# Optimization experiments

Measured on AMD Instinct MI355X. Metric: run time of the kernel, lower is better.

## Reference

```python
import jax, jax.numpy as jnp
import numpy as np


def setup_inputs() -> dict:
    key = jax.random.key(0)
    k1, k2 = jax.random.split(key)
    B, C, T = 16, 256, 1500
    K = 2048
    x = jax.random.normal(k1, (B, C, T), dtype=jnp.float32)
    # torch init: uniform(-1/K, 1/K)
    codebook = jax.random.uniform(k2, (K, C), dtype=jnp.float32,
                                  minval=-1.0 / K, maxval=1.0 / K)
    return {"x": x, "codebook": codebook}


def reference(x, codebook):
    B, C, T = x.shape
    # (B, T, C) -> (B*T, C)
    x_flat = jnp.transpose(x, (0, 2, 1)).reshape(-1, C)
    distances = (jnp.sum(x_flat * x_flat, axis=1, keepdims=True)
                 - 2.0 * x_flat @ codebook.T
                 + jnp.sum(codebook * codebook, axis=1))  # (B*T, K)
    indices = jnp.argmin(distances, axis=1)               # (B*T,)
    quantized_flat = codebook[indices]                    # (B*T, C)
    quantized = jnp.transpose(quantized_flat.reshape(B, T, C), (0, 2, 1))
    indices_out = indices.reshape(B, 1, T)
    # straight-through estimator
    quantized_out = x + jax.lax.stop_gradient(quantized - x)
    commitment_loss = jnp.mean((jax.lax.stop_gradient(quantized) - x) ** 2)
    return quantized_out, indices_out, commitment_loss
```

## Files before the change

kernel.cpp:

```cpp
#include <hip/hip_runtime.h>


#define B_DIM 16
#define C_DIM 256
#define T_DIM 1500
#define K_CODES 2048
#define N_ROWS (B_DIM * T_DIM)
#define TOTAL_ELEMS (B_DIM * C_DIM * T_DIM)

#define TM 32
#define TKC 256
#define CS 32
#define OT 64

__global__ __launch_bounds__(256) void vq_se(const float* __restrict__ cb,
                                             float* __restrict__ Se) {
    const int k = blockIdx.x * 256 + threadIdx.x;
    if (k >= K_CODES) return;
    const float* row = cb + (size_t)k * C_DIM;
    float h[2];
#pragma unroll
    for (int half = 0; half < 2; ++half) {
        const float* a = row + half * 128;
        float r[8];
#pragma unroll
        for (int j = 0; j < 8; ++j) r[j] = __fmul_rn(a[j], a[j]);
        for (int i = 8; i < 128; i += 8)
#pragma unroll
            for (int j = 0; j < 8; ++j)
                r[j] = __fadd_rn(r[j], __fmul_rn(a[i + j], a[i + j]));
        h[half] = __fadd_rn(
            __fadd_rn(__fadd_rn(r[0], r[1]), __fadd_rn(r[2], r[3])),
            __fadd_rn(__fadd_rn(r[4], r[5]), __fadd_rn(r[6], r[7])));
    }
    Se[k] = __fadd_rn(h[0], h[1]);
}

__global__ __launch_bounds__(256) void vq_sx(const float* __restrict__ x,
                                             float* __restrict__ Sx) {
    const int n = blockIdx.x * 256 + threadIdx.x;
    if (n >= N_ROWS) return;
    const int b = n / T_DIM, t = n - b * T_DIM;
    const float* base = x + (size_t)b * C_DIM * T_DIM + t;
    float h[2];
#pragma unroll
    for (int half = 0; half < 2; ++half) {
        float r[8];
#pragma unroll
        for (int j = 0; j < 8; ++j) {
            const float v = base[(size_t)(half * 128 + j) * T_DIM];
            r[j] = __fmul_rn(v, v);
        }
        for (int i = 8; i < 128; i += 8)
#pragma unroll
            for (int j = 0; j < 8; ++j) {
                const float v = base[(size_t)(half * 128 + i + j) * T_DIM];
                r[j] = __fadd_rn(r[j], __fmul_rn(v, v));
            }
        h[half] = __fadd_rn(
            __fadd_rn(__fadd_rn(r[0], r[1]), __fadd_rn(r[2], r[3])),
            __fadd_rn(__fadd_rn(r[4], r[5]), __fadd_rn(r[6], r[7])));
    }
    Sx[n] = __fadd_rn(h[0], h[1]);
}

__global__ __launch_bounds__(256) void vq_argmin(
    const float* __restrict__ x, const float* __restrict__ cb,
    const float* __restrict__ Se, const float* __restrict__ Sx,
    int* __restrict__ idxws) {
    __shared__ float xs[TM * CS];
    __shared__ float cs[TKC * CS];
    __shared__ float e2s[TKC];
    __shared__ float Sxs[TM];

    const int tid = threadIdx.x;
    const int b = blockIdx.y;
    const int t0 = blockIdx.x * TM;

    const int tr = tid & 7;
    const int tcol = tid >> 3;

    if (tid < TM) {
        const int t = t0 + tid;
        Sxs[tid] = (t < T_DIM) ? Sx[b * T_DIM + t] : 0.f;
    }

    float m1[4];
    int k1r[4];
#pragma unroll
    for (int i = 0; i < 4; ++i) { m1[i] = 1e30f; k1r[i] = 0; }

    for (int kc = 0; kc < K_CODES; kc += TKC) {
        __syncthreads();
        e2s[tid] = Se[kc + tid];

        float acc[4][8];
#pragma unroll
        for (int i = 0; i < 4; ++i)
#pragma unroll
            for (int j = 0; j < 8; ++j) acc[i][j] = 0.f;

        for (int c0 = 0; c0 < C_DIM; c0 += CS) {
            __syncthreads();
            {
                const int tq = tid & 7;
                const int ci = tid >> 3;
                const int t = t0 + tq * 4;
                float4 v = make_float4(0.f, 0.f, 0.f, 0.f);
                if (t < T_DIM)
                    v = *reinterpret_cast<const float4*>(
                        x + (size_t)(b * C_DIM + c0 + ci) * T_DIM + t);
                const int gc = ci >> 2, w = ci & 3;
                const int swg = ((gc ^ tq) << 2) | w;
#pragma unroll
                for (int q = 0; q < 4; ++q)
                    xs[(tq * 4 + q) * CS + swg] = (&v.x)[q];
            }
            {
#pragma unroll
                for (int p = 0; p < 8; ++p) {
                    const int id = tid + (p << 8);
                    const int kk = id >> 3;
                    const int g4 = id & 7;
                    const float4 v = *reinterpret_cast<const float4*>(
                        cb + (size_t)(kc + kk) * C_DIM + c0 + g4 * 4);
                    *reinterpret_cast<float4*>(
                        &cs[kk * CS + ((g4 ^ ((kk >> 3) & 7)) << 2)]) = v;
                }
            }
            __syncthreads();
#pragma unroll
            for (int g = 0; g < 8; ++g) {
                float4 xv[4];
#pragma unroll
                for (int i = 0; i < 4; ++i)
                    xv[i] = *reinterpret_cast<const float4*>(
                        &xs[(tr * 4 + i) * CS + ((g ^ tr) << 2)]);
#pragma unroll
                for (int j = 0; j < 8; ++j) {
                    const int kk = tcol * 8 + j;
                    const float4 cv = *reinterpret_cast<const float4*>(
                        &cs[kk * CS + ((g ^ (tcol & 7)) << 2)]);
#pragma unroll
                    for (int i = 0; i < 4; ++i) {
                        acc[i][j] = fmaf(xv[i].x, cv.x, acc[i][j]);
                        acc[i][j] = fmaf(xv[i].y, cv.y, acc[i][j]);
                        acc[i][j] = fmaf(xv[i].z, cv.z, acc[i][j]);
                        acc[i][j] = fmaf(xv[i].w, cv.w, acc[i][j]);
                    }
                }
            }
        }
#pragma unroll
        for (int j = 0; j < 8; ++j) {
            const int kk = tcol * 8 + j;
            const float ev = e2s[kk];
            const int kglob = kc + kk;
#pragma unroll
            for (int i = 0; i < 4; ++i) {
                const float twoM = __fmul_rn(2.0f, acc[i][j]);
                const float s = __fadd_rn(__fsub_rn(Sxs[tr * 4 + i], twoM), ev);
                if (s < m1[i]) { m1[i] = s; k1r[i] = kglob; }
            }
        }
    }

    __syncthreads();
    float* redm1 = cs;
    int* redk1 = reinterpret_cast<int*>(cs + TM * 32);
#pragma unroll
    for (int i = 0; i < 4; ++i) {
        const int r = tr * 4 + i;
        redm1[r * 32 + tcol] = m1[i];
        redk1[r * 32 + tcol] = k1r[i];
    }
    __syncthreads();
    if (tid < TM) {
        const int r = tid;
        float bm1 = 1e30f;
        int bk = 0x7fffffff;
        for (int tc = 0; tc < 32; ++tc) {
            const float c1 = redm1[r * 32 + tc];
            const int ck = redk1[r * 32 + tc];
            if (c1 < bm1 || (c1 == bm1 && ck < bk)) { bm1 = c1; bk = ck; }
        }
        const int t = t0 + r;
        if (t < T_DIM) idxws[b * T_DIM + t] = bk;
    }
}

__global__ __launch_bounds__(256) void vq_output(
    const float* __restrict__ x, const float* __restrict__ cb,
    const int* __restrict__ idxws, float* __restrict__ out,
    float* __restrict__ partials) {
    const int tid = threadIdx.x;
    const int b = blockIdx.y;
    const int t0 = blockIdx.x * OT;
    __shared__ int idxs[OT];
    if (tid < OT) {
        const int t = t0 + tid;
        if (t < T_DIM) {
            const int id = idxws[b * T_DIM + t];
            idxs[tid] = id;
            out[(size_t)TOTAL_ELEMS + b * T_DIM + t] = (float)id;
        }
    }
    __syncthreads();
    const int ti = tid & 63;
    const int cq = tid >> 6;
    const int t = t0 + ti;
    float lsum = 0.f;
    if (t < T_DIM) {
        const int id = idxs[ti];
        for (int c0 = 0; c0 < C_DIM; c0 += 4) {
            const int c = c0 + cq;
            const size_t off = (size_t)(b * C_DIM + c) * T_DIM + t;
            const float xv = x[off];
            const float q = cb[(size_t)id * C_DIM + c];
            out[off] = __fadd_rn(xv, __fsub_rn(q, xv));
            const float d = __fsub_rn(q, xv);
            lsum = fmaf(d, d, lsum);
        }
    }
#pragma unroll
    for (int off = 32; off; off >>= 1) lsum += __shfl_down(lsum, off, 64);
    __shared__ float wsum[4];
    if ((tid & 63) == 0) wsum[tid >> 6] = lsum;
    __syncthreads();
    if (tid == 0)
        partials[blockIdx.y * gridDim.x + blockIdx.x] =
            wsum[0] + wsum[1] + wsum[2] + wsum[3];
}

__global__ void vq_loss(const float* __restrict__ partials, int nparts,
                        float* __restrict__ out) {
    __shared__ float red[256];
    float s = 0.f;
    for (int i = threadIdx.x; i < nparts; i += 256) s += partials[i];
    red[threadIdx.x] = s;
    __syncthreads();
    for (int off = 128; off; off >>= 1) {
        if (threadIdx.x < off) red[threadIdx.x] += red[threadIdx.x + off];
        __syncthreads();
    }
    if (threadIdx.x == 0)
        out[(size_t)TOTAL_ELEMS + N_ROWS] = red[0] * (1.0f / (float)TOTAL_ELEMS);
}

extern "C" void kernel_launch(void* const* d_in, const int* in_sizes, int n_in,
                              void* d_out, int out_size, void* d_ws, size_t ws_size,
                              hipStream_t stream) {
    const float* x = (const float*)d_in[0];
    const float* cb = (const float*)d_in[1];
    float* out = (float*)d_out;

    float* Se = (float*)d_ws;
    float* Sx = Se + K_CODES;
    int* idxws = (int*)d_ws + K_CODES + N_ROWS;
    float* partials = (float*)d_ws + K_CODES + 2 * N_ROWS;

    vq_se<<<dim3((K_CODES + 255) / 256), dim3(256), 0, stream>>>(cb, Se);
    vq_sx<<<dim3((N_ROWS + 255) / 256), dim3(256), 0, stream>>>(x, Sx);
    vq_argmin<<<dim3((T_DIM + TM - 1) / TM, B_DIM), dim3(256), 0, stream>>>(
        x, cb, Se, Sx, idxws);
    vq_output<<<dim3((T_DIM + OT - 1) / OT, B_DIM), dim3(256), 0, stream>>>(
        x, cb, idxws, out, partials);
    vq_loss<<<dim3(1), dim3(256), 0, stream>>>(
        partials, (T_DIM + OT - 1) / OT * B_DIM, out);
}
```

Measured before the change: 480.1 us.

## Split codebook across blocks, pre-transpose x, use direct LDS loads and 8x8 tiles

Adds a transpose kernel that writes x as (B,T,C) into the output buffer as scratch, so row loads are contiguous and can use global_load_lds straight into swizzled shared memory. The argmin kernel now computes an 8x8 register tile per thread over 64 rows and splits K into four slices across grid z. Partial minima are merged with a packed 64-bit atomicMin, which relies on all distances being non-negative. The aim is more parallelism and more FMAs per shared-memory load, at the cost of extra transpose traffic, atomics and higher register pressure.

```diff
diff --git a/kernel.cpp b/kernel.cpp
--- a/kernel.cpp
+++ b/kernel.cpp
@@ -1,4 +1,5 @@
 #include <hip/hip_runtime.h>
+#include <stdint.h>
 
 
 #define B_DIM 16
@@ -8,10 +9,40 @@
 #define N_ROWS (B_DIM * T_DIM)
 #define TOTAL_ELEMS (B_DIM * C_DIM * T_DIM)
 
-#define TM 32
+#define TM 64
 #define TKC 256
 #define CS 32
+#define KSLICE 512
 #define OT 64
+
+__device__ __forceinline__ void gl_lds16(const float* g, float* l) {
+    __builtin_amdgcn_global_load_lds(
+        (const __attribute__((address_space(1))) void*)(uintptr_t)g,
+        (__attribute__((address_space(3))) void*)(uintptr_t)l, 16, 0, 0);
+}
+
+__global__ __launch_bounds__(256) void vq_transpose(const float* __restrict__ x,
+                                                    float* __restrict__ xT) {
+    __shared__ float tile[32][33];
+    const int b = blockIdx.z;
+    const int t0 = blockIdx.x * 32;
+    const int c0 = blockIdx.y * 32;
+    const int tx = threadIdx.x & 31;
+    const int ty = threadIdx.x >> 5;
+#pragma unroll
+    for (int q = 0; q < 4; ++q) {
+        const int c = c0 + ty * 4 + q;
+        int t = t0 + tx; if (t >= T_DIM) t = T_DIM - 1;
+        tile[ty * 4 + q][tx] = x[((size_t)b * C_DIM + c) * T_DIM + t];
+    }
+    __syncthreads();
+#pragma unroll
+    for (int q = 0; q < 4; ++q) {
+        const int t = t0 + ty * 4 + q;
+        if (t < T_DIM)
+            xT[((size_t)b * T_DIM + t) * C_DIM + c0 + tx] = tile[tx][ty * 4 + q];
+    }
+}
 
 __global__ __launch_bounds__(256) void vq_se(const float* __restrict__ cb,
                                              float* __restrict__ Se) {
@@ -36,27 +67,22 @@
     Se[k] = __fadd_rn(h[0], h[1]);
 }
 
-__global__ __launch_bounds__(256) void vq_sx(const float* __restrict__ x,
+__global__ __launch_bounds__(256) void vq_sx(const float* __restrict__ xT,
                                              float* __restrict__ Sx) {
     const int n = blockIdx.x * 256 + threadIdx.x;
     if (n >= N_ROWS) return;
-    const int b = n / T_DIM, t = n - b * T_DIM;
-    const float* base = x + (size_t)b * C_DIM * T_DIM + t;
+    const float* row = xT + (size_t)n * C_DIM;
     float h[2];
 #pragma unroll
     for (int half = 0; half < 2; ++half) {
+        const float* a = row + half * 128;
         float r[8];
 #pragma unroll
-        for (int j = 0; j < 8; ++j) {
-            const float v = base[(size_t)(half * 128 + j) * T_DIM];
-            r[j] = __fmul_rn(v, v);
-        }
+        for (int j = 0; j < 8; ++j) r[j] = __fmul_rn(a[j], a[j]);
         for (int i = 8; i < 128; i += 8)
 #pragma unroll
-            for (int j = 0; j < 8; ++j) {
-                const float v = base[(size_t)(half * 128 + i + j) * T_DIM];
-                r[j] = __fadd_rn(r[j], __fmul_rn(v, v));
-            }
+            for (int j = 0; j < 8; ++j)
+                r[j] = __fadd_rn(r[j], __fmul_rn(a[i + j], a[i + j]));
         h[half] = __fadd_rn(
             __fadd_rn(__fadd_rn(r[0], r[1]), __fadd_rn(r[2], r[3])),
             __fadd_rn(__fadd_rn(r[4], r[5]), __fadd_rn(r[6], r[7])));
@@ -64,134 +90,133 @@
     Sx[n] = __fadd_rn(h[0], h[1]);
 }
 
+__global__ void vq_init(unsigned long long* __restrict__ slots) {
+    const int n = blockIdx.x * 256 + threadIdx.x;
+    if (n < N_ROWS) slots[n] = ~0ull;
+}
+
 __global__ __launch_bounds__(256) void vq_argmin(
-    const float* __restrict__ x, const float* __restrict__ cb,
+    const float* __restrict__ xT, const float* __restrict__ cb,
     const float* __restrict__ Se, const float* __restrict__ Sx,
-    int* __restrict__ idxws) {
+    unsigned long long* __restrict__ slots) {
     __shared__ float xs[TM * CS];
     __shared__ float cs[TKC * CS];
     __shared__ float e2s[TKC];
     __shared__ float Sxs[TM];
 
     const int tid = threadIdx.x;
+    const int t0 = blockIdx.x * TM;
     const int b = blockIdx.y;
-    const int t0 = blockIdx.x * TM;
-
+    const int k0 = blockIdx.z * KSLICE;
     const int tr = tid & 7;
     const int tcol = tid >> 3;
 
     if (tid < TM) {
-        const int t = t0 + tid;
+        int t = t0 + tid;
         Sxs[tid] = (t < T_DIM) ? Sx[b * T_DIM + t] : 0.f;
     }
 
-    float m1[4];
-    int k1r[4];
-#pragma unroll
-    for (int i = 0; i < 4; ++i) { m1[i] = 1e30f; k1r[i] = 0; }
-
-    for (int kc = 0; kc < K_CODES; kc += TKC) {
+    float m1[8];
+    int k1[8];
+#pragma unroll
+    for (int i = 0; i < 8; ++i) { m1[i] = 1e30f; k1[i] = 0x7fffffff; }
+
+    const float* xTb = xT + (size_t)b * T_DIM * C_DIM;
+
+    for (int kc = 0; kc < KSLICE; kc += TKC) {
         __syncthreads();
-        e2s[tid] = Se[kc + tid];
-
-        float acc[4][8];
-#pragma unroll
-        for (int i = 0; i < 4; ++i)
+        e2s[tid] = Se[k0 + kc + tid];
+
+        float acc[8][8];
+#pragma unroll
+        for (int i = 0; i < 8; ++i)
 #pragma unroll
             for (int j = 0; j < 8; ++j) acc[i][j] = 0.f;
 
         for (int c0 = 0; c0 < C_DIM; c0 += CS) {
             __syncthreads();
-            {
-                const int tq = tid & 7;
-                const int ci = tid >> 3;
-                const int t = t0 + tq * 4;
-                float4 v = make_float4(0.f, 0.f, 0.f, 0.f);
-                if (t < T_DIM)
-                    v = *reinterpret_cast<const float4*>(
-                        x + (size_t)(b * C_DIM + c0 + ci) * T_DIM + t);
-                const int gc = ci >> 2, w = ci & 3;
-                const int swg = ((gc ^ tq) << 2) | w;
-#pragma unroll
-                for (int q = 0; q < 4; ++q)
-                    xs[(tq * 4 + q) * CS + swg] = (&v.x)[q];
+#pragma unroll
+            for (int p = 0; p < 2; ++p) {
+                const int A = p * 256 + tid;
+                const int r = A >> 3, slot = A & 7;
+                const int g4 = slot ^ ((r >> 3) & 7);
+                int t = t0 + r; if (t >= T_DIM) t = T_DIM - 1;
+                gl_lds16(xTb + (size_t)t * C_DIM + c0 + g4 * 4, &xs[A * 4]);
             }
-            {
-#pragma unroll
-                for (int p = 0; p < 8; ++p) {
-                    const int id = tid + (p << 8);
-                    const int kk = id >> 3;
-                    const int g4 = id & 7;
-                    const float4 v = *reinterpret_cast<const float4*>(
-                        cb + (size_t)(kc + kk) * C_DIM + c0 + g4 * 4);
-                    *reinterpret_cast<float4*>(
-                        &cs[kk * CS + ((g4 ^ ((kk >> 3) & 7)) << 2)]) = v;
-                }
+#pragma unroll
+            for (int i = 0; i < 8; ++i) {
+                const int A = i * 256 + tid;
+                const int kk = A >> 3, slot = A & 7;
+                const int g4 = slot ^ ((kk >> 3) & 7);
+                gl_lds16(cb + (size_t)(k0 + kc + kk) * C_DIM + c0 + g4 * 4,
+                         &cs[A * 4]);
             }
             __syncthreads();
 #pragma unroll
             for (int g = 0; g < 8; ++g) {
-                float4 xv[4];
-#pragma unroll
-                for (int i = 0; i < 4; ++i)
-                    xv[i] = *reinterpret_cast<const float4*>(
-                        &xs[(tr * 4 + i) * CS + ((g ^ tr) << 2)]);
-#pragma unroll
-                for (int j = 0; j < 8; ++j) {
-                    const int kk = tcol * 8 + j;
-                    const float4 cv = *reinterpret_cast<const float4*>(
-                        &cs[kk * CS + ((g ^ (tcol & 7)) << 2)]);
-#pragma unroll
-                    for (int i = 0; i < 4; ++i) {
-                        acc[i][j] = fmaf(xv[i].x, cv.x, acc[i][j]);
-                        acc[i][j] = fmaf(xv[i].y, cv.y, acc[i][j]);
-                        acc[i][j] = fmaf(xv[i].z, cv.z, acc[i][j]);
-                        acc[i][j] = fmaf(xv[i].w, cv.w, acc[i][j]);
+                float4 cv[8];
+#pragma unroll
+                for (int j = 0; j < 8; ++j)
+                    cv[j] = *reinterpret_cast<const float4*>(
+                        &cs[(tcol * 8 + j) * CS + ((g ^ (tcol & 7)) << 2)]);
+#pragma unroll
+                for (int i = 0; i < 8; ++i) {
+                    const float4 xv = *reinterpret_cast<const float4*>(
+                        &xs[(tr * 8 + i) * CS + ((g ^ tr) << 2)]);
+#pragma unroll
+                    for (int j = 0; j < 8; ++j) {
+                        acc[i][j] = fmaf(xv.x, cv[j].x, acc[i][j]);
+                        acc[i][j] = fmaf(xv.y, cv[j].y, acc[i][j]);
+                        acc[i][j] = fmaf(xv.z, cv[j].z, acc[i][j]);
+                        acc[i][j] = fmaf(xv.w, cv[j].w, acc[i][j]);
                     }
                 }
             }
         }
 #pragma unroll
         for (int j = 0; j < 8; ++j) {
-            const int kk = tcol * 8 + j;
-            const float ev = e2s[kk];
-            const int kglob = kc + kk;
-#pragma unroll
-            for (int i = 0; i < 4; ++i) {
-                const float twoM = __fmul_rn(2.0f, acc[i][j]);
-                const float s = __fadd_rn(__fsub_rn(Sxs[tr * 4 + i], twoM), ev);
-                if (s < m1[i]) { m1[i] = s; k1r[i] = kglob; }
+            const float ev = e2s[tcol * 8 + j];
+            const int kg = k0 + kc + tcol * 8 + j;
+#pragma unroll
+            for (int i = 0; i < 8; ++i) {
+                const float s = __fadd_rn(
+                    __fsub_rn(Sxs[tr * 8 + i], __fmul_rn(2.0f, acc[i][j])), ev);
+                if (s < m1[i]) { m1[i] = s; k1[i] = kg; }
             }
         }
     }
 
     __syncthreads();
-    float* redm1 = cs;
-    int* redk1 = reinterpret_cast<int*>(cs + TM * 32);
-#pragma unroll
-    for (int i = 0; i < 4; ++i) {
-        const int r = tr * 4 + i;
-        redm1[r * 32 + tcol] = m1[i];
-        redk1[r * 32 + tcol] = k1r[i];
+    float* redm = cs;
+    int* redk = reinterpret_cast<int*>(cs + TM * 32);
+#pragma unroll
+    for (int i = 0; i < 8; ++i) {
+        const int r = tr * 8 + i;
+        redm[r * 32 + tcol] = m1[i];
+        redk[r * 32 + tcol] = k1[i];
     }
     __syncthreads();
     if (tid < TM) {
         const int r = tid;
-        float bm1 = 1e30f;
+        float bm = 1e30f;
         int bk = 0x7fffffff;
         for (int tc = 0; tc < 32; ++tc) {
-            const float c1 = redm1[r * 32 + tc];
-            const int ck = redk1[r * 32 + tc];
-            if (c1 < bm1 || (c1 == bm1 && ck < bk)) { bm1 = c1; bk = ck; }
+            const float c1 = redm[r * 32 + tc];
+            const int ck = redk[r * 32 + tc];
+            if (c1 < bm || (c1 == bm && ck < bk)) { bm = c1; bk = ck; }
         }
         const int t = t0 + r;
-        if (t < T_DIM) idxws[b * T_DIM + t] = bk;
+        if (t < T_DIM) {
+            const unsigned long long pack =
+                ((unsigned long long)__float_as_uint(bm) << 32) | (unsigned)bk;
+            atomicMin(slots + b * T_DIM + t, pack);
+        }
     }
 }
 
 __global__ __launch_bounds__(256) void vq_output(
     const float* __restrict__ x, const float* __restrict__ cb,
-    const int* __restrict__ idxws, float* __restrict__ out,
+    const unsigned long long* __restrict__ slots, float* __restrict__ out,
     float* __restrict__ partials) {
     const int tid = threadIdx.x;
     const int b = blockIdx.y;
@@ -200,7 +225,7 @@
     if (tid < OT) {
         const int t = t0 + tid;
         if (t < T_DIM) {
-            const int id = idxws[b * T_DIM + t];
+            const int id = (int)(unsigned)(slots[b * T_DIM + t] & 0xffffffffull);
             idxs[tid] = id;
             out[(size_t)TOTAL_ELEMS + b * T_DIM + t] = (float)id;
         }
@@ -254,17 +279,22 @@
     const float* cb = (const float*)d_in[1];
     float* out = (float*)d_out;
 
+    float* xT = out;
+
     float* Se = (float*)d_ws;
     float* Sx = Se + K_CODES;
-    int* idxws = (int*)d_ws + K_CODES + N_ROWS;
-    float* partials = (float*)d_ws + K_CODES + 2 * N_ROWS;
-
-    vq_se<<<dim3((K_CODES + 255) / 256), dim3(256), 0, stream>>>(cb, Se);
-    vq_sx<<<dim3((N_ROWS + 255) / 256), dim3(256), 0, stream>>>(x, Sx);
-    vq_argmin<<<dim3((T_DIM + TM - 1) / TM, B_DIM), dim3(256), 0, stream>>>(
-        x, cb, Se, Sx, idxws);
+    unsigned long long* slots =
+        (unsigned long long*)((char*)d_ws + ((8192 + 96000 + 7) & ~7ull));
+    float* partials = (float*)(slots + N_ROWS);
+
+    vq_transpose<<<dim3(47, 8, B_DIM), dim3(256), 0, stream>>>(x, xT);
+    vq_se<<<dim3(K_CODES / 256), dim3(256), 0, stream>>>(cb, Se);
+    vq_sx<<<dim3((N_ROWS + 255) / 256), dim3(256), 0, stream>>>(xT, Sx);
+    vq_init<<<dim3((N_ROWS + 255) / 256), dim3(256), 0, stream>>>(slots);
+    vq_argmin<<<dim3((T_DIM + TM - 1) / TM, B_DIM, K_CODES / KSLICE),
+                dim3(256), 0, stream>>>(xT, cb, Se, Sx, slots);
     vq_output<<<dim3((T_DIM + OT - 1) / OT, B_DIM), dim3(256), 0, stream>>>(
-        x, cb, idxws, out, partials);
+        x, cb, slots, out, partials);
     vq_loss<<<dim3(1), dim3(256), 0, stream>>>(
         partials, (T_DIM + OT - 1) / OT * B_DIM, out);
 }
```

Measured after the change: 387.2 us. -19.4%, faster.
